# Performance work log

Hardware: AMD Instinct MI355X
Metric: run time of the kernel (lower is better)

The kernel has to match this reference:

```python
import jax, jax.numpy as jnp
import numpy as np
import math

HIDDEN = 512
NUM_HEADS = 16
HEAD_DIM = HIDDEN // NUM_HEADS          # 32
SPOW_DIM = HEAD_DIM * (HEAD_DIM + 1) // 2  # 528
GAMMA = 0.9
B, S = 2, 1024

_TRIU_I, _TRIU_J = np.triu_indices(HEAD_DIM, k=1)
_SQRT2 = math.sqrt(2.0)


def spow2(x):
    # x: (..., d) -> (..., d*(d+1)//2); squares then sqrt(2)*upper-tri cross terms
    squares = x * x
    cross = _SQRT2 * (x[..., _TRIU_I] * x[..., _TRIU_J])
    return jnp.concatenate([squares, cross], axis=-1)


def setup_inputs() -> dict:
    key = jax.random.key(0)
    ks = jax.random.split(key, 9)
    lim = 1.0 / math.sqrt(HIDDEN)
    w = lambda k: jax.random.uniform(k, (HIDDEN, HIDDEN), jnp.float32, -lim, lim)
    b = lambda k: jax.random.uniform(k, (HIDDEN,), jnp.float32, -lim, lim)
    return {
        "x": jax.random.normal(ks[0], (B, S, HIDDEN), jnp.float32),
        "q_w": w(ks[1]), "q_b": b(ks[2]),
        "k_w": w(ks[3]), "k_b": b(ks[4]),
        "v_w": w(ks[5]), "v_b": b(ks[6]),
        "o_w": w(ks[7]), "o_b": b(ks[8]),
    }


def reference(x, q_w, q_b, k_w, k_b, v_w, v_b, o_w, o_b):
    Bb, Ss, Hh = x.shape
    q = (x @ q_w + q_b).reshape(Bb, Ss, NUM_HEADS, HEAD_DIM)
    k = (x @ k_w + k_b).reshape(Bb, Ss, NUM_HEADS, HEAD_DIM)
    v = (x @ v_w + v_b).reshape(Bb, Ss, NUM_HEADS, HEAD_DIM)

    sq = spow2(q)  # [B,S,H,Dspow]
    sk = spow2(k)  # [B,S,H,Dspow]

    # time-major for scan
    sq_t = jnp.moveaxis(sq, 1, 0)  # [S,B,H,D]
    sk_t = jnp.moveaxis(sk, 1, 0)
    v_t = jnp.moveaxis(v, 1, 0)    # [S,B,H,hd]

    state0 = jnp.zeros((Bb, NUM_HEADS, SPOW_DIM, HEAD_DIM), x.dtype)

    def step(state, inp):
        skt, sqt, vt = inp
        # state = gamma*state + spow_k \otimes v  -> [B,H,Dspow,hd]
        state = GAMMA * state + skt[..., :, None] * vt[..., None, :]
        out = jnp.einsum('bhD,bhDd->bhd', sqt, state)
        return state, out

    _, outs = jax.lax.scan(step, state0, (sk_t, sq_t, v_t))  # [S,B,H,hd]
    out = jnp.moveaxis(outs, 0, 1).reshape(Bb, Ss, Hh)
    return out @ o_w + o_b
```

## Files before the change

### kernel.cpp

```cpp
#include <hip/hip_runtime.h>
#include <hip/hip_bf16.h>
#include <math.h>

#define HIDDEN 512
#define NHEADS 16
#define HDIM   32
#define BATCH  2
#define SEQ    1024
#define MROWS  (BATCH * SEQ)

constexpr float LOG2_GAMMA = -0.15200309344504997f;

typedef __hip_bfloat16 bf16;
typedef __attribute__((ext_vector_type(8))) short short8;
typedef __attribute__((ext_vector_type(4))) float f32x4;

__device__ __forceinline__ unsigned short f2bf_bits(float f) {
    bf16 b = __float2bfloat16(f);
    return *(unsigned short*)&b;
}

__global__ __launch_bounds__(256) void prep(
    const float* __restrict__ x,
    const float* __restrict__ qw, const float* __restrict__ kw,
    const float* __restrict__ vw, const float* __restrict__ ow,
    bf16* __restrict__ xb, bf16* __restrict__ wqkvt, bf16* __restrict__ wot)
{
    const int blk = blockIdx.x, tid = threadIdx.x;
    if (blk < 256) {
        const int widx = blk >> 6;
        const int tile = blk & 63;
        const int tk = (tile & 7) * 64, tn = (tile >> 3) * 64;
        const float* w = widx == 0 ? qw : widx == 1 ? kw : widx == 2 ? vw : ow;
        __shared__ float t[64][65];
        #pragma unroll
        for (int u = 0; u < 4; ++u) {
            const int r = u * 16 + (tid >> 4);
            const int c = (tid & 15) * 4;
            float4 v = *(const float4*)&w[(size_t)(tk + r) * 512 + tn + c];
            t[r][c + 0] = v.x; t[r][c + 1] = v.y; t[r][c + 2] = v.z; t[r][c + 3] = v.w;
        }
        __syncthreads();
        #pragma unroll
        for (int u = 0; u < 2; ++u) {
            const int rr = u * 32 + (tid >> 3);
            const int cc = (tid & 7) * 8;
            alignas(16) unsigned short tmp[8];
            #pragma unroll
            for (int i = 0; i < 8; ++i) tmp[i] = f2bf_bits(t[cc + i][rr]);
            bf16* dst = (widx < 3)
                ? &wqkvt[((size_t)widx * 512 + tn + rr) * 512 + tk + cc]
                : &wot[(size_t)(tn + rr) * 512 + tk + cc];
            *(short8*)dst = *(short8*)tmp;
        }
    } else {
        #pragma unroll
        for (int u = 0; u < 4; ++u) {
            const int idx = (blk - 256) * 1024 + u * 256 + tid;
            float4 v = ((const float4*)x)[idx];
            unsigned pk0 = (unsigned)f2bf_bits(v.x) | ((unsigned)f2bf_bits(v.y) << 16);
            unsigned pk1 = (unsigned)f2bf_bits(v.z) | ((unsigned)f2bf_bits(v.w) << 16);
            uint2 pk = {pk0, pk1};
            *(uint2*)&xb[(size_t)idx * 4] = pk;
        }
    }
}

template<int EPI>
__global__ __launch_bounds__(256) void gemm_direct(
    const bf16* __restrict__ A, const bf16* __restrict__ Bt,
    const float* __restrict__ b0, const float* __restrict__ b1,
    const float* __restrict__ b2,
    float* __restrict__ Cf, bf16* __restrict__ Cb, int ldc)
{
    constexpr int K = 512;
    const int tid = threadIdx.x;
    const int wave = tid >> 6, lane = tid & 63;
    const int fr = lane & 15, quad = lane >> 4;
    const int m0 = blockIdx.y * 64 + (wave >> 1) * 32;
    const int n0 = blockIdx.x * 64 + (wave & 1) * 32;

    const bf16* pa0 = &A[(size_t)(m0 + fr) * K + quad * 8];
    const bf16* pa1 = pa0 + (size_t)16 * K;
    const bf16* pb0 = &Bt[(size_t)(n0 + fr) * K + quad * 8];
    const bf16* pb1 = pb0 + (size_t)16 * K;

    f32x4 acc00 = {}, acc01 = {}, acc10 = {}, acc11 = {};
    short8 ca0 = *(const short8*)pa0;
    short8 ca1 = *(const short8*)pa1;
    short8 cb0 = *(const short8*)pb0;
    short8 cb1 = *(const short8*)pb1;

    #pragma unroll
    for (int ks = 0; ks < 16; ++ks) {
        short8 na0, na1, nb0, nb1;
        if (ks < 15) {
            na0 = *(const short8*)(pa0 + (ks + 1) * 32);
            na1 = *(const short8*)(pa1 + (ks + 1) * 32);
            nb0 = *(const short8*)(pb0 + (ks + 1) * 32);
            nb1 = *(const short8*)(pb1 + (ks + 1) * 32);
        }
        acc00 = __builtin_amdgcn_mfma_f32_16x16x32_bf16(ca0, cb0, acc00, 0, 0, 0);
        acc01 = __builtin_amdgcn_mfma_f32_16x16x32_bf16(ca0, cb1, acc01, 0, 0, 0);
        acc10 = __builtin_amdgcn_mfma_f32_16x16x32_bf16(ca1, cb0, acc10, 0, 0, 0);
        acc11 = __builtin_amdgcn_mfma_f32_16x16x32_bf16(ca1, cb1, acc11, 0, 0, 0);
        ca0 = na0; ca1 = na1; cb0 = nb0; cb1 = nb1;
    }

    f32x4 acc[2][2] = {{acc00, acc01}, {acc10, acc11}};

    if (EPI == 1) {
        const int seg = (blockIdx.x * 64) >> 9;
        const float* bp = seg == 0 ? b0 : seg == 1 ? b1 : b2;
        const float sgn = seg == 0 ? 0.5f : seg == 1 ? -0.5f : 0.0f;
        #pragma unroll
        for (int i = 0; i < 2; ++i) {
            const int mrow = m0 + i * 16 + quad * 4;
            float sc[4];
            #pragma unroll
            for (int r = 0; r < 4; ++r)
                sc[r] = exp2f((float)((mrow + r) & 63) * (sgn * LOG2_GAMMA));
            #pragma unroll
            for (int j = 0; j < 2; ++j) {
                const int n = n0 + j * 16 + fr;
                const float bv = bp[n & 511];
                #pragma unroll
                for (int r = 0; r < 4; ++r) {
                    unsigned short h = f2bf_bits((acc[i][j][r] + bv) * sc[r]);
                    *(unsigned short*)&Cb[(size_t)(mrow + r) * ldc + n] = h;
                }
            }
        }
    } else {
        #pragma unroll
        for (int i = 0; i < 2; ++i) {
            const int mrow = m0 + i * 16 + quad * 4;
            #pragma unroll
            for (int j = 0; j < 2; ++j) {
                const int n = n0 + j * 16 + fr;
                const float bv = b0[n];
                #pragma unroll
                for (int r = 0; r < 4; ++r)
                    Cf[(size_t)(mrow + r) * ldc + n] = acc[i][j][r] + bv;
            }
        }
    }
}

__global__ __launch_bounds__(256) void power_attn_mfma(
    const bf16* __restrict__ qkv, bf16* __restrict__ atc)
{
    __shared__ alignas(16) short Vt[32 * 80];
    __shared__ alignas(16) short Ps[64 * 72];

    const int tid = threadIdx.x, wave = tid >> 6, lane = tid & 63;
    const int chunk = blockIdx.x, bh = blockIdx.y;
    const int b = bh >> 4, h = bh & 15;
    const int mb = b * SEQ + chunk * 64;
    const int fr = lane & 15, quad = lane >> 4;

    short8 aq = *(const short8*)&qkv[(size_t)(mb + wave * 16 + fr) * 1536 + h * 32 + quad * 8];

    f32x4 o0 = {}, o1 = {};
    const int jstart = chunk >= 2 ? chunk - 2 : 0;

    for (int j = jstart; j <= chunk; ++j) {
        __syncthreads();
        const int sb = b * SEQ + j * 64;
        if (tid < 128) {
            const int p = tid >> 2, s = p * 2, dbase = (tid & 3) * 8;
            const short* g = (const short*)&qkv[(size_t)(sb + s) * 1536 + 1024 + h * 32 + dbase];
            short8 v0 = *(const short8*)g;
            short8 v1 = *(const short8*)(g + 1536);
            #pragma unroll
            for (int i = 0; i < 8; ++i) {
                unsigned pk = (unsigned)(unsigned short)v0[i]
                            | ((unsigned)(unsigned short)v1[i] << 16);
                *(unsigned*)&Vt[(dbase + i) * 80 + s] = pk;
            }
        }
        __syncthreads();

        f32x4 sAcc[4] = {};
        #pragma unroll
        for (int nt = 0; nt < 4; ++nt) {
            short8 bk = *(const short8*)&qkv[(size_t)(sb + nt * 16 + fr) * 1536 + 512 + h * 32 + quad * 8];
            sAcc[nt] = __builtin_amdgcn_mfma_f32_16x16x32_bf16(aq, bk, sAcc[nt], 0, 0, 0);
        }

        const int dj = chunk - j;
        const float sj = exp2f(64.0f * (float)dj * LOG2_GAMMA);
        const int tbase = wave * 16 + quad * 4;
        #pragma unroll
        for (int nt = 0; nt < 4; ++nt) {
            const int s_l = nt * 16 + fr;
            #pragma unroll
            for (int r = 0; r < 4; ++r) {
                const int t_l = tbase + r;
                float pv = sAcc[nt][r];
                pv = pv * pv * sj;
                if (dj == 0 && s_l > t_l) pv = 0.0f;
                Ps[t_l * 72 + s_l] = (short)f2bf_bits(pv);
            }
        }
        short8 a0 = *(const short8*)&Ps[(wave * 16 + fr) * 72 + quad * 8];
        short8 a1 = *(const short8*)&Ps[(wave * 16 + fr) * 72 + 32 + quad * 8];
        short8 b00 = *(const short8*)&Vt[fr * 80 + quad * 8];
        short8 b01 = *(const short8*)&Vt[fr * 80 + 32 + quad * 8];
        short8 b10 = *(const short8*)&Vt[(16 + fr) * 80 + quad * 8];
        short8 b11 = *(const short8*)&Vt[(16 + fr) * 80 + 32 + quad * 8];
        o0 = __builtin_amdgcn_mfma_f32_16x16x32_bf16(a0, b00, o0, 0, 0, 0);
        o0 = __builtin_amdgcn_mfma_f32_16x16x32_bf16(a1, b01, o0, 0, 0, 0);
        o1 = __builtin_amdgcn_mfma_f32_16x16x32_bf16(a0, b10, o1, 0, 0, 0);
        o1 = __builtin_amdgcn_mfma_f32_16x16x32_bf16(a1, b11, o1, 0, 0, 0);
    }

    #pragma unroll
    for (int r = 0; r < 4; ++r) {
        const size_t row = mb + wave * 16 + quad * 4 + r;
        const int col = h * 32 + fr;
        *(unsigned short*)&atc[row * 512 + col]      = f2bf_bits(o0[r]);
        *(unsigned short*)&atc[row * 512 + col + 16] = f2bf_bits(o1[r]);
    }
}

extern "C" void kernel_launch(void* const* d_in, const int* in_sizes, int n_in,
                              void* d_out, int out_size, void* d_ws, size_t ws_size,
                              hipStream_t stream)
{
    const float* x  = (const float*)d_in[0];
    const float* qw = (const float*)d_in[1];
    const float* qb = (const float*)d_in[2];
    const float* kw = (const float*)d_in[3];
    const float* kb = (const float*)d_in[4];
    const float* vw = (const float*)d_in[5];
    const float* vb = (const float*)d_in[6];
    const float* ow = (const float*)d_in[7];
    const float* ob = (const float*)d_in[8];
    float* out = (float*)d_out;

    char* w = (char*)d_ws;
    bf16* xb    = (bf16*)(w);
    bf16* wqkvt = (bf16*)(w + (2ull  << 20));
    bf16* wot   = (bf16*)(w + (2ull  << 20) + (1536ull << 10));
    bf16* qkvb  = (bf16*)(w + (4ull  << 20));
    bf16* atc   = (bf16*)(w + (10ull << 20));

    prep<<<512, 256, 0, stream>>>(x, qw, kw, vw, ow, xb, wqkvt, wot);

    gemm_direct<1><<<dim3(1536 / 64, MROWS / 64), 256, 0, stream>>>(
        xb, wqkvt, qb, kb, vb, nullptr, qkvb, 1536);

    power_attn_mfma<<<dim3(SEQ / 64, BATCH * NHEADS), 256, 0, stream>>>(qkvb, atc);

    gemm_direct<0><<<dim3(512 / 64, MROWS / 64), 256, 0, stream>>>(
        atc, wot, ob, nullptr, nullptr, out, nullptr, 512);
}
```

Baseline: 115.2 us.

## Stage GEMM and attention K/V tiles in LDS via async global-to-LDS loads

```diff
diff --git a/kernel.cpp b/kernel.cpp
--- a/kernel.cpp
+++ b/kernel.cpp
@@ -14,6 +14,12 @@
 typedef __hip_bfloat16 bf16;
 typedef __attribute__((ext_vector_type(8))) short short8;
 typedef __attribute__((ext_vector_type(4))) float f32x4;
+
+__device__ __forceinline__ void async16(const void* g, void* l) {
+    __builtin_amdgcn_global_load_lds(
+        (const __attribute__((address_space(1))) void*)g,
+        (__attribute__((address_space(3))) void*)l, 16, 0, 0);
+}
 
 __device__ __forceinline__ unsigned short f2bf_bits(float f) {
     bf16 b = __float2bfloat16(f);
@@ -67,77 +73,92 @@
 }
 
 template<int EPI>
-__global__ __launch_bounds__(256) void gemm_direct(
+__global__ __launch_bounds__(256) void gemm_tile64(
     const bf16* __restrict__ A, const bf16* __restrict__ Bt,
     const float* __restrict__ b0, const float* __restrict__ b1,
     const float* __restrict__ b2,
     float* __restrict__ Cf, bf16* __restrict__ Cb, int ldc)
 {
     constexpr int K = 512;
+    __shared__ alignas(16) short As[64 * 256];
+    __shared__ alignas(16) short Bs[64 * 256];
+
     const int tid = threadIdx.x;
     const int wave = tid >> 6, lane = tid & 63;
     const int fr = lane & 15, quad = lane >> 4;
-    const int m0 = blockIdx.y * 64 + (wave >> 1) * 32;
-    const int n0 = blockIdx.x * 64 + (wave & 1) * 32;
-
-    const bf16* pa0 = &A[(size_t)(m0 + fr) * K + quad * 8];
-    const bf16* pa1 = pa0 + (size_t)16 * K;
-    const bf16* pb0 = &Bt[(size_t)(n0 + fr) * K + quad * 8];
-    const bf16* pb1 = pb0 + (size_t)16 * K;
-
-    f32x4 acc00 = {}, acc01 = {}, acc10 = {}, acc11 = {};
-    short8 ca0 = *(const short8*)pa0;
-    short8 ca1 = *(const short8*)pa1;
-    short8 cb0 = *(const short8*)pb0;
-    short8 cb1 = *(const short8*)pb1;
+    const int m0 = blockIdx.y * 64, n0 = blockIdx.x * 64;
+    const int wm = (wave >> 1) * 32, wn = (wave & 1) * 32;
+
+    const int rl = lane >> 5;
+    const int chs = lane & 31;
+
+    const int ar0 = wm + fr, ar1 = ar0 + 16;
+    const int br0 = wn + fr, br1 = br0 + 16;
+    const char* cA0 = (const char*)&As[ar0 * 256];
+    const char* cA1 = (const char*)&As[ar1 * 256];
+    const char* cB0 = (const char*)&Bs[br0 * 256];
+    const char* cB1 = (const char*)&Bs[br1 * 256];
+    const int xa0 = (ar0 & 7) * 16, xa1 = (ar1 & 7) * 16;
+    const int xb0 = (br0 & 7) * 16, xb1 = (br1 & 7) * 16;
+
+    f32x4 acc[2][2] = {};
 
     #pragma unroll
-    for (int ks = 0; ks < 16; ++ks) {
-        short8 na0, na1, nb0, nb1;
-        if (ks < 15) {
-            na0 = *(const short8*)(pa0 + (ks + 1) * 32);
-            na1 = *(const short8*)(pa1 + (ks + 1) * 32);
-            nb0 = *(const short8*)(pb0 + (ks + 1) * 32);
-            nb1 = *(const short8*)(pb1 + (ks + 1) * 32);
-        }
-        acc00 = __builtin_amdgcn_mfma_f32_16x16x32_bf16(ca0, cb0, acc00, 0, 0, 0);
-        acc01 = __builtin_amdgcn_mfma_f32_16x16x32_bf16(ca0, cb1, acc01, 0, 0, 0);
-        acc10 = __builtin_amdgcn_mfma_f32_16x16x32_bf16(ca1, cb0, acc10, 0, 0, 0);
-        acc11 = __builtin_amdgcn_mfma_f32_16x16x32_bf16(ca1, cb1, acc11, 0, 0, 0);
-        ca0 = na0; ca1 = na1; cb0 = nb0; cb1 = nb1;
-    }
-
-    f32x4 acc[2][2] = {{acc00, acc01}, {acc10, acc11}};
+    for (int kk = 0; kk < 2; ++kk) {
+        if (kk) __syncthreads();
+        #pragma unroll
+        for (int j = 0; j < 8; ++j) {
+            const int r0 = wave * 16 + j * 2;
+            const int row = r0 + rl;
+            const int g = chs ^ (row & 7);
+            async16(&A[(size_t)(m0 + row) * K + kk * 256 + g * 8], &As[r0 * 256]);
+            async16(&Bt[(size_t)(n0 + row) * K + kk * 256 + g * 8], &Bs[r0 * 256]);
+        }
+        __syncthreads();
+
+        #pragma unroll
+        for (int ks = 0; ks < 8; ++ks) {
+            const int cb = (ks * 4 + quad) * 16;
+            short8 a0 = *(const short8*)(cA0 + (cb ^ xa0));
+            short8 a1 = *(const short8*)(cA1 + (cb ^ xa1));
+            short8 q0 = *(const short8*)(cB0 + (cb ^ xb0));
+            short8 q1 = *(const short8*)(cB1 + (cb ^ xb1));
+            acc[0][0] = __builtin_amdgcn_mfma_f32_16x16x32_bf16(a0, q0, acc[0][0], 0, 0, 0);
+            acc[0][1] = __builtin_amdgcn_mfma_f32_16x16x32_bf16(a0, q1, acc[0][1], 0, 0, 0);
+            acc[1][0] = __builtin_amdgcn_mfma_f32_16x16x32_bf16(a1, q0, acc[1][0], 0, 0, 0);
+            acc[1][1] = __builtin_amdgcn_mfma_f32_16x16x32_bf16(a1, q1, acc[1][1], 0, 0, 0);
+        }
+    }
 
     if (EPI == 1) {
-        const int seg = (blockIdx.x * 64) >> 9;
+        const int seg = n0 >> 9;
         const float* bp = seg == 0 ? b0 : seg == 1 ? b1 : b2;
         const float sgn = seg == 0 ? 0.5f : seg == 1 ? -0.5f : 0.0f;
         #pragma unroll
         for (int i = 0; i < 2; ++i) {
-            const int mrow = m0 + i * 16 + quad * 4;
+            const int mrow = m0 + wm + i * 16 + quad * 4;
             float sc[4];
             #pragma unroll
             for (int r = 0; r < 4; ++r)
                 sc[r] = exp2f((float)((mrow + r) & 63) * (sgn * LOG2_GAMMA));
             #pragma unroll
             for (int j = 0; j < 2; ++j) {
-                const int n = n0 + j * 16 + fr;
+                const int n = n0 + wn + j * 16 + fr;
                 const float bv = bp[n & 511];
                 #pragma unroll
                 for (int r = 0; r < 4; ++r) {
-                    unsigned short h = f2bf_bits((acc[i][j][r] + bv) * sc[r]);
-                    *(unsigned short*)&Cb[(size_t)(mrow + r) * ldc + n] = h;
+                    unsigned short hh = f2bf_bits((acc[i][j][r] + bv) * sc[r]);
+                    *(unsigned short*)&Cb[(size_t)(mrow + r) * ldc + n] = hh;
                 }
             }
         }
     } else {
         #pragma unroll
         for (int i = 0; i < 2; ++i) {
-            const int mrow = m0 + i * 16 + quad * 4;
+            const int mrow = m0 + wm + i * 16 + quad * 4;
             #pragma unroll
             for (int j = 0; j < 2; ++j) {
-                const int n = n0 + j * 16 + fr;
+                const int n = n0 + wn + j * 16 + fr;
                 const float bv = b0[n];
                 #pragma unroll
                 for (int r = 0; r < 4; ++r)
@@ -150,7 +171,8 @@
 __global__ __launch_bounds__(256) void power_attn_mfma(
     const bf16* __restrict__ qkv, bf16* __restrict__ atc)
 {
-    __shared__ alignas(16) short Vt[32 * 80];
+    __shared__ alignas(16) short Ks[3][64 * 32];
+    __shared__ alignas(16) short Vt[3][32 * 80];
     __shared__ alignas(16) short Ps[64 * 72];
 
     const int tid = threadIdx.x, wave = tid >> 6, lane = tid & 63;
@@ -158,17 +180,25 @@
     const int b = bh >> 4, h = bh & 15;
     const int mb = b * SEQ + chunk * 64;
     const int fr = lane & 15, quad = lane >> 4;
+    const int jstart = chunk >= 2 ? chunk - 2 : 0;
+    const int cnt = chunk - jstart + 1;
 
     short8 aq = *(const short8*)&qkv[(size_t)(mb + wave * 16 + fr) * 1536 + h * 32 + quad * 8];
 
-    f32x4 o0 = {}, o1 = {};
-    const int jstart = chunk >= 2 ? chunk - 2 : 0;
-
-    for (int j = jstart; j <= chunk; ++j) {
-        __syncthreads();
-        const int sb = b * SEQ + j * 64;
-        if (tid < 128) {
-            const int p = tid >> 2, s = p * 2, dbase = (tid & 3) * 8;
+    const int srow = lane >> 2;
+    const int sg = (lane & 3) ^ (srow & 3);
+    for (int jj = 0; jj < cnt; ++jj) {
+        const int sb = b * SEQ + (jstart + jj) * 64;
+        async16(&qkv[(size_t)(sb + wave * 16 + srow) * 1536 + 512 + h * 32 + sg * 8],
+                &Ks[jj][wave * 512]);
+    }
+    #pragma unroll
+    for (int u = 0; u < 2; ++u) {
+        const int task = tid + u * 256;
+        if (task < cnt * 128) {
+            const int jj = task >> 7, tt = task & 127;
+            const int s = (tt >> 2) * 2, dbase = (tt & 3) * 8;
+            const int sb = b * SEQ + (jstart + jj) * 64;
             const short* g = (const short*)&qkv[(size_t)(sb + s) * 1536 + 1024 + h * 32 + dbase];
             short8 v0 = *(const short8*)g;
             short8 v1 = *(const short8*)(g + 1536);
@@ -176,19 +206,25 @@
             for (int i = 0; i < 8; ++i) {
                 unsigned pk = (unsigned)(unsigned short)v0[i]
                             | ((unsigned)(unsigned short)v1[i] << 16);
-                *(unsigned*)&Vt[(dbase + i) * 80 + s] = pk;
-            }
-        }
-        __syncthreads();
-
+                *(unsigned*)&Vt[jj][(dbase + i) * 80 + s] = pk;
+            }
+        }
+    }
+    __syncthreads();
+
+    f32x4 o0 = {}, o1 = {};
+
+    for (int jj = 0; jj < cnt; ++jj) {
         f32x4 sAcc[4] = {};
         #pragma unroll
         for (int nt = 0; nt < 4; ++nt) {
-            short8 bk = *(const short8*)&qkv[(size_t)(sb + nt * 16 + fr) * 1536 + 512 + h * 32 + quad * 8];
+            const int krow = nt * 16 + fr;
+            short8 bk = *(const short8*)((const char*)&Ks[jj][0]
+                          + krow * 64 + ((quad * 16) ^ ((fr & 3) * 16)));
             sAcc[nt] = __builtin_amdgcn_mfma_f32_16x16x32_bf16(aq, bk, sAcc[nt], 0, 0, 0);
         }
 
-        const int dj = chunk - j;
+        const int dj = cnt - 1 - jj;
         const float sj = exp2f(64.0f * (float)dj * LOG2_GAMMA);
         const int tbase = wave * 16 + quad * 4;
         #pragma unroll
@@ -205,10 +241,10 @@
         }
         short8 a0 = *(const short8*)&Ps[(wave * 16 + fr) * 72 + quad * 8];
         short8 a1 = *(const short8*)&Ps[(wave * 16 + fr) * 72 + 32 + quad * 8];
-        short8 b00 = *(const short8*)&Vt[fr * 80 + quad * 8];
-        short8 b01 = *(const short8*)&Vt[fr * 80 + 32 + quad * 8];
-        short8 b10 = *(const short8*)&Vt[(16 + fr) * 80 + quad * 8];
-        short8 b11 = *(const short8*)&Vt[(16 + fr) * 80 + 32 + quad * 8];
+        short8 b00 = *(const short8*)&Vt[jj][fr * 80 + quad * 8];
+        short8 b01 = *(const short8*)&Vt[jj][fr * 80 + 32 + quad * 8];
+        short8 b10 = *(const short8*)&Vt[jj][(16 + fr) * 80 + quad * 8];
+        short8 b11 = *(const short8*)&Vt[jj][(16 + fr) * 80 + 32 + quad * 8];
         o0 = __builtin_amdgcn_mfma_f32_16x16x32_bf16(a0, b00, o0, 0, 0, 0);
         o0 = __builtin_amdgcn_mfma_f32_16x16x32_bf16(a1, b01, o0, 0, 0, 0);
         o1 = __builtin_amdgcn_mfma_f32_16x16x32_bf16(a0, b10, o1, 0, 0, 0);
@@ -248,11 +284,11 @@
 
     prep<<<512, 256, 0, stream>>>(x, qw, kw, vw, ow, xb, wqkvt, wot);
 
-    gemm_direct<1><<<dim3(1536 / 64, MROWS / 64), 256, 0, stream>>>(
+    gemm_tile64<1><<<dim3(1536 / 64, MROWS / 64), 256, 0, stream>>>(
         xb, wqkvt, qb, kb, vb, nullptr, qkvb, 1536);
 
     power_attn_mfma<<<dim3(SEQ / 64, BATCH * NHEADS), 256, 0, stream>>>(qkvb, atc);
 
-    gemm_direct<0><<<dim3(512 / 64, MROWS / 64), 256, 0, stream>>>(
+    gemm_tile64<0><<<dim3(512 / 64, MROWS / 64), 256, 0, stream>>>(
         atc, wot, ob, nullptr, nullptr, out, nullptr, 512);
 }
```

Result: faster. 99.00 us (-14.0%).
